# Performance work log

Hardware: AMD Instinct MI355X
Metric: run time of the kernel (lower is better)

The kernel has to match this reference:

```python
import jax, jax.numpy as jnp
import numpy as np
import math

B, T, C, H = 2, 2048, 1024, 16
HD = C // H  # head dim = 64

def setup_inputs() -> dict:
    key = jax.random.key(0)
    ks = jax.random.split(key, 12)
    s = 0.02
    return {
        "x": jax.random.normal(ks[0], (B, T, C), dtype=jnp.float32),
        "ln1_g": jnp.ones((C,), jnp.float32),
        "ln1_b": jnp.zeros((C,), jnp.float32),
        "W_attn": jax.random.normal(ks[1], (C, 3 * C), jnp.float32) * s,
        "b_attn": jnp.zeros((3 * C,), jnp.float32),
        "W_ap": jax.random.normal(ks[2], (C, C), jnp.float32) * s,
        "b_ap": jnp.zeros((C,), jnp.float32),
        "ln2_g": jnp.ones((C,), jnp.float32),
        "ln2_b": jnp.zeros((C,), jnp.float32),
        "W_fc": jax.random.normal(ks[3], (C, 4 * C), jnp.float32) * s,
        "b_fc": jnp.zeros((4 * C,), jnp.float32),
        "W_mp": jax.random.normal(ks[4], (4 * C, C), jnp.float32) * s,
        "b_mp": jnp.zeros((C,), jnp.float32),
    }

def layernorm(x, g, b, eps=1e-5):
    mu = jnp.mean(x, axis=-1, keepdims=True)
    var = jnp.mean(jnp.square(x - mu), axis=-1, keepdims=True)
    return (x - mu) * jax.lax.rsqrt(var + eps) * g + b

def gelu_tanh(x):
    # GELU(approximate='tanh')
    c = math.sqrt(2.0 / math.pi)
    return 0.5 * x * (1.0 + jnp.tanh(c * (x + 0.044715 * x * x * x)))

def attention(x, W_attn, b_attn, W_ap, b_ap):
    b, t, c = x.shape
    qkv = x @ W_attn + b_attn                      # [B,T,3C]
    q, k, v = jnp.split(qkv, 3, axis=-1)
    q = q.reshape(b, t, H, HD).transpose(0, 2, 1, 3)  # [B,H,T,hd]
    k = k.reshape(b, t, H, HD).transpose(0, 2, 1, 3)
    v = v.reshape(b, t, H, HD).transpose(0, 2, 1, 3)
    attn = jnp.einsum('bhqd,bhkd->bhqk', q, k) * (1.0 / math.sqrt(HD))
    mask = jnp.tril(jnp.ones((t, t), dtype=bool))
    attn = jnp.where(mask, attn, jnp.float32(-jnp.inf))
    attn = jax.nn.softmax(attn, axis=-1)
    y = jnp.einsum('bhqk,bhkd->bhqd', attn, v)
    y = y.transpose(0, 2, 1, 3).reshape(b, t, c)
    return y @ W_ap + b_ap

def reference(x, ln1_g, ln1_b, W_attn, b_attn, W_ap, b_ap,
              ln2_g, ln2_b, W_fc, b_fc, W_mp, b_mp):
    x = x + attention(layernorm(x, ln1_g, ln1_b), W_attn, b_attn, W_ap, b_ap)
    h = layernorm(x, ln2_g, ln2_b)
    h = gelu_tanh(h @ W_fc + b_fc) @ W_mp + b_mp
    return x + h
```

## Files before the change

### kernel.cpp

```cpp
#include <hip/hip_runtime.h>
#include <stdint.h>

#define TT_ 2048
#define CC_ 1024

typedef unsigned short u16;
typedef __bf16 bf16x8 __attribute__((ext_vector_type(8)));
typedef float f32x4 __attribute__((ext_vector_type(4)));
typedef unsigned short u16x8 __attribute__((ext_vector_type(8)));
typedef unsigned int u32x2 __attribute__((ext_vector_type(2)));

__device__ __forceinline__ u16 f2bf(float f) {
  unsigned u = __float_as_uint(f);
  u += 0x7fff + ((u >> 16) & 1);
  return (u16)(u >> 16);
}
__device__ __forceinline__ float bf2f(u16 v) {
  return __uint_as_float(((unsigned)v) << 16);
}

__device__ __forceinline__ float gelu_f(float t) {
  float u = 1.5957691216057308f * (t + 0.044715f * t * t * t);
  return t / (1.f + __expf(-u));
}

__device__ __forceinline__ void async_cp16(const u16* g, u16* l) {
  __builtin_amdgcn_global_load_lds(
      (const __attribute__((address_space(1))) void*)(uintptr_t)g,
      (__attribute__((address_space(3))) void*)(uint32_t)(uintptr_t)l,
      16, 0, 0);
}

__device__ __forceinline__ void blockbar() {
  asm volatile("" ::: "memory");
  __builtin_amdgcn_s_barrier();
  asm volatile("" ::: "memory");
}

__global__ __launch_bounds__(256) void kconv_t(const float* __restrict__ W,
                                               u16* __restrict__ WT, int K, int N) {
  __shared__ float t[32][33];
  int n0 = blockIdx.x * 32, k0 = blockIdx.y * 32;
  int tx = threadIdx.x & 31, ty = threadIdx.x >> 5;
#pragma unroll
  for (int r = 0; r < 4; ++r)
    t[ty + 8 * r][tx] = W[(size_t)(k0 + ty + 8 * r) * N + n0 + tx];
  __syncthreads();
#pragma unroll
  for (int r = 0; r < 4; ++r)
    WT[(size_t)(n0 + ty + 8 * r) * K + k0 + tx] = f2bf(t[tx][ty + 8 * r]);
}

__global__ __launch_bounds__(256) void kln(const float* __restrict__ x,
                                           const float* __restrict__ g,
                                           const float* __restrict__ b,
                                           u16* __restrict__ out) {
  int row = blockIdx.x, tid = threadIdx.x;
  const float4* xr = (const float4*)(x + (size_t)row * CC_);
  float4 v = xr[tid];
  float s = v.x + v.y + v.z + v.w;
  float s2 = v.x * v.x + v.y * v.y + v.z * v.z + v.w * v.w;
#pragma unroll
  for (int off = 32; off; off >>= 1) { s += __shfl_down(s, off); s2 += __shfl_down(s2, off); }
  __shared__ float rs[4], rq[4];
  int w = tid >> 6;
  if ((tid & 63) == 0) { rs[w] = s; rq[w] = s2; }
  __syncthreads();
  s = rs[0] + rs[1] + rs[2] + rs[3];
  s2 = rq[0] + rq[1] + rq[2] + rq[3];
  float mean = s * (1.f / CC_);
  float var = s2 * (1.f / CC_) - mean * mean;
  float rstd = rsqrtf(var + 1e-5f);
  float4 gv = ((const float4*)g)[tid];
  float4 bv = ((const float4*)b)[tid];
  u16* orow = out + (size_t)row * CC_ + tid * 4;
  orow[0] = f2bf((v.x - mean) * rstd * gv.x + bv.x);
  orow[1] = f2bf((v.y - mean) * rstd * gv.y + bv.y);
  orow[2] = f2bf((v.z - mean) * rstd * gv.z + bv.z);
  orow[3] = f2bf((v.w - mean) * rstd * gv.w + bv.w);
}

template <int EPI, int NSPLIT>
__global__ __launch_bounds__(256) void kgemm(const u16* __restrict__ A,
                                             const u16* __restrict__ BTm,
                                             const float* __restrict__ bias,
                                             const float* __restrict__ resid,
                                             void* __restrict__ out,
                                             float* __restrict__ part,
                                             int M, int N, int Ktot) {
  __shared__ __align__(16) u16 As[2][128 * 32];
  __shared__ __align__(16) u16 Bs[2][128 * 32];
  const int tid = threadIdx.x, lane = tid & 63, w = tid >> 6;
  const int llo = lane & 15, lhi = lane >> 4;
  const int row0 = blockIdx.y * 128, col0 = blockIdx.x * 128;
  const int wr = w >> 1, wc = w & 1;
  const int crow = lane >> 2;
  const int ck = (lane & 3) * 8;
  const int Kc = Ktot / NSPLIT;
  const int klo = (NSPLIT > 1) ? blockIdx.z * Kc : 0;

  f32x4 acc[4][4] = {};

  auto stage = [&](int bufi, int kof) {
#pragma unroll
    for (int c = w; c < 8; c += 4) {
      int r = c * 16 + crow;
      async_cp16(A + (size_t)(row0 + r) * Ktot + klo + kof + ck, &As[bufi][c * 512]);
      async_cp16(BTm + (size_t)(col0 + r) * Ktot + klo + kof + ck, &Bs[bufi][c * 512]);
    }
  };

  const int nt = Kc / 32;
  stage(0, 0);
  asm volatile("s_waitcnt vmcnt(0)" ::: "memory");
  blockbar();
  int cur = 0;

  for (int t = 0; t < nt; ++t) {
    if (t + 1 < nt) stage(cur ^ 1, (t + 1) * 32);
    bf16x8 af[4], bfr[4];
#pragma unroll
    for (int m = 0; m < 4; ++m)
      af[m] = *(const bf16x8*)&As[cur][(wr * 64 + m * 16 + llo) * 32 + lhi * 8];
#pragma unroll
    for (int n = 0; n < 4; ++n)
      bfr[n] = *(const bf16x8*)&Bs[cur][(wc * 64 + n * 16 + llo) * 32 + lhi * 8];
#pragma unroll
    for (int m = 0; m < 4; ++m)
#pragma unroll
      for (int n = 0; n < 4; ++n)
        acc[m][n] = __builtin_amdgcn_mfma_f32_16x16x32_bf16(af[m], bfr[n], acc[m][n], 0, 0, 0);
    if (t + 1 < nt) {
      asm volatile("s_waitcnt vmcnt(0)" ::: "memory");
      blockbar();
    }
    cur ^= 1;
  }

  const int c_row = row0 + wr * 64 + lhi * 4;
  const int c_col = col0 + wc * 64 + llo;
  const bool fin = (NSPLIT == 1) || (blockIdx.z == 0);
#pragma unroll
  for (int n = 0; n < 4; ++n) {
    int col = c_col + n * 16;
    float bb = bias[col];
#pragma unroll
    for (int m = 0; m < 4; ++m) {
      f32x4 a = acc[m][n];
#pragma unroll
      for (int i = 0; i < 4; ++i) {
        size_t idx = (size_t)(c_row + m * 16 + i) * N + col;
        if (!fin) {
          part[idx] = a[i];
        } else {
          float val = a[i] + bb;
          if constexpr (EPI == 1) {
            ((float*)out)[idx] = val + resid[idx];
          } else if constexpr (EPI == 2) {
            ((u16*)out)[idx] = f2bf(gelu_f(val));
          } else {
            ((u16*)out)[idx] = f2bf(val);
          }
        }
      }
    }
  }
}

template <int EPI, int NSPLIT>
__global__ __launch_bounds__(512, 2) void kgemm2(const u16* __restrict__ A,
                                                 const u16* __restrict__ BTm,
                                                 const float* __restrict__ bias,
                                                 const float* __restrict__ resid,
                                                 void* __restrict__ out,
                                                 u16* __restrict__ part,
                                                 int M, int N, int Ktot) {
  __shared__ __align__(16) u16 LB[4][2][8192];
  const int tid = threadIdx.x, lane = tid & 63, w = tid >> 6;
  const int llo = lane & 15, lhi = lane >> 4;
  const int wr = w >> 2, wc = w & 3;
  const int row0 = blockIdx.y * 256, col0 = blockIdx.x * 256;
  const int Kc = Ktot / NSPLIT;
  const int klo = (NSPLIT > 1) ? blockIdx.z * Kc : 0;
  const int nt = Kc / 32;

  const int wsA = w & 3;
  const int hbB = (wc >> 1);
  const int wsB = (w & 1) + ((w >> 2) << 1);

  const u16 *gA[2], *gB[2];
  int ldsA[2], ldsB[2];
#pragma unroll
  for (int l = 0; l < 2; ++l) {
    int c = l * 256 + wsA * 64 + lane;
    int rowl = c >> 2;
    int kc = ((c & 3) ^ ((c >> 3) & 3)) * 8;
    gA[l] = A + (size_t)(row0 + wr * 128 + rowl) * Ktot + klo + kc;
    ldsA[l] = wr * 4096 + (l * 256 + wsA * 64) * 8;
    int c2 = l * 256 + wsB * 64 + lane;
    int row2 = c2 >> 2;
    int kc2 = ((c2 & 3) ^ ((c2 >> 3) & 3)) * 8;
    gB[l] = BTm + (size_t)(col0 + hbB * 128 + row2) * Ktot + klo + kc2;
    ldsB[l] = hbB * 4096 + (l * 256 + wsB * 64) * 8;
  }

  auto stage = [&](int t) {
    int slot = t & 3;
#pragma unroll
    for (int l = 0; l < 2; ++l) {
      async_cp16(gA[l] + (size_t)t * 32, &LB[slot][0][ldsA[l]]);
      async_cp16(gB[l] + (size_t)t * 32, &LB[slot][1][ldsB[l]]);
    }
  };

  f32x4 acc[8][4] = {};
  for (int t = 0; t < 3 && t < nt; ++t) stage(t);
  const int swz = (llo >> 1) & 3;
  const int aoffb = wr * 4096 + llo * 32 + (lhi ^ swz) * 8;
  const int boffb = hbB * 4096 + ((wc & 1) * 64 + llo) * 32 + (lhi ^ swz) * 8;

  for (int t = 0; t < nt; ++t) {
    const int slot = t & 3;
    const int rem = nt - 1 - t;
    if (rem >= 2)      asm volatile("s_waitcnt vmcnt(8)" ::: "memory");
    else if (rem == 1) asm volatile("s_waitcnt vmcnt(4)" ::: "memory");
    else               asm volatile("s_waitcnt vmcnt(0)" ::: "memory");
    asm volatile("s_waitcnt lgkmcnt(0)" ::: "memory");
    blockbar();
    if (t + 3 < nt) stage(t + 3);

    bf16x8 af[8], bfv[4];
#pragma unroll
    for (int n = 0; n < 4; ++n)
      bfv[n] = *(const bf16x8*)&LB[slot][1][boffb + n * 512];
#pragma unroll
    for (int m = 0; m < 8; ++m)
      af[m] = *(const bf16x8*)&LB[slot][0][aoffb + m * 512];
    __builtin_amdgcn_s_setprio(1);
#pragma unroll
    for (int m = 0; m < 8; ++m)
#pragma unroll
      for (int n = 0; n < 4; ++n)
        acc[m][n] = __builtin_amdgcn_mfma_f32_16x16x32_bf16(af[m], bfv[n], acc[m][n], 0, 0, 0);
    __builtin_amdgcn_s_setprio(0);
  }

  const int c_row0 = row0 + wr * 128 + lhi * 4;
  const int c_col0 = col0 + wc * 64 + llo;
  const bool fin = (NSPLIT == 1) || (blockIdx.z == 0);
  u16* pb = part + (NSPLIT > 1 ? ((size_t)(blockIdx.z - 1)) * M * N : 0);
#pragma unroll
  for (int n = 0; n < 4; ++n) {
    int col = c_col0 + n * 16;
    float bb = bias[col];
#pragma unroll
    for (int m = 0; m < 8; ++m) {
      f32x4 a = acc[m][n];
#pragma unroll
      for (int i = 0; i < 4; ++i) {
        size_t idx = (size_t)(c_row0 + m * 16 + i) * N + col;
        if (!fin) {
          pb[idx] = f2bf(a[i]);
        } else {
          float val = a[i] + bb;
          if constexpr (EPI == 1) {
            ((float*)out)[idx] = val + resid[idx];
          } else if constexpr (EPI == 2) {
            ((u16*)out)[idx] = f2bf(gelu_f(val));
          } else {
            ((u16*)out)[idx] = f2bf(val);
          }
        }
      }
    }
  }
}

__global__ __launch_bounds__(256) void kadd3(float* __restrict__ out,
                                             const u16* __restrict__ p, size_t MN) {
  size_t i0 = ((size_t)blockIdx.x * 256 + threadIdx.x) * 8;
  float4 o0 = *(float4*)(out + i0);
  float4 o1 = *(float4*)(out + i0 + 4);
#pragma unroll
  for (int s = 0; s < 3; ++s) {
    u16x8 v = *(const u16x8*)(p + s * MN + i0);
    o0.x += bf2f(v[0]); o0.y += bf2f(v[1]); o0.z += bf2f(v[2]); o0.w += bf2f(v[3]);
    o1.x += bf2f(v[4]); o1.y += bf2f(v[5]); o1.z += bf2f(v[6]); o1.w += bf2f(v[7]);
  }
  *(float4*)(out + i0) = o0;
  *(float4*)(out + i0 + 4) = o1;
}

__global__ __launch_bounds__(256) void kvtrans(const u16* __restrict__ qkv,
                                               u16* __restrict__ VT) {
  int tt = blockIdx.x;
  int bh = blockIdx.y;
  int b = bh >> 4, h = bh & 15;
  __shared__ u16 t[64][72];
  int r = threadIdx.x >> 3, c0 = (threadIdx.x & 7) * 8;
  const u16* src = qkv + (size_t)(b * TT_ + tt * 64) * 3072 + 2048 + h * 64;
#pragma unroll
  for (int it = 0; it < 2; ++it) {
    int rr = r + it * 32;
    *(u16x8*)&t[rr][c0] = *(const u16x8*)(src + (size_t)rr * 3072 + c0);
  }
  __syncthreads();
  u16* dst = VT + ((size_t)bh * 64) * TT_ + tt * 64;
#pragma unroll
  for (int it = 0; it < 2; ++it) {
    int d = r + it * 32;
    u16x8 v;
#pragma unroll
    for (int e = 0; e < 8; ++e) v[e] = t[c0 + e][d];
    *(u16x8*)(dst + (size_t)d * TT_ + c0) = v;
  }
}

__global__ __launch_bounds__(512, 4) void kattn(const u16* __restrict__ qkv,
                                                const u16* __restrict__ VT,
                                                u16* __restrict__ y) {
  const int h = blockIdx.x, b = blockIdx.y;
  const int z = blockIdx.z;
  const int qt = (z < 8) ? (15 - z) : (z - 8);
  const int tid = threadIdx.x, lane = tid & 63, w = tid >> 6;
  const int llo = lane & 15, lhi = lane >> 4;

  __shared__ __align__(16) u16 Qs[128 * 64];
  __shared__ __align__(16) u16 Ks[2][64 * 64];
  __shared__ __align__(16) u16 Vs[2][64 * 64];
  __shared__ __align__(16) u16 Ps[128 * 72];

  const size_t tok0 = (size_t)b * TT_;
  const int q0 = qt * 128;
  const u16* qb = qkv + tok0 * 3072 + h * 64;
  const u16* kb = qb + 1024;

  {
    const float alpha = 0.18033688011112042f;
    int r8 = tid >> 3, ce = (tid & 7) * 8;
#pragma unroll
    for (int it = 0; it < 2; ++it) {
      int tk = it * 64 + r8;
      u16x8 v = *(const u16x8*)(qb + (size_t)(q0 + tk) * 3072 + ce);
#pragma unroll
      for (int e = 0; e < 8; ++e) v[e] = f2bf(bf2f(v[e]) * alpha);
      *(u16x8*)&Qs[tk * 64 + (ce ^ ((tk & 7) << 3))] = v;
    }
  }
  asm volatile("s_waitcnt lgkmcnt(0)" ::: "memory");

  const int p_ = w * 8 + (lane >> 3);
  const int krow = ((p_ & 15) << 2) | (p_ >> 4);
  const int scol = ((lane & 7) * 8) ^ ((p_ & 7) << 3);
  const u16* kg = kb + (size_t)krow * 3072 + scol;
  const u16* vg = VT + ((size_t)(b * 16 + h) * 64 + p_) * TT_ + scol;

  const int ntiles = 2 * qt + 2;
  async_cp16(kg, &Ks[0][w * 512]);
  async_cp16(vg, &Vs[0][w * 512]);

  blockbar();

  bf16x8 aq[2];
#pragma unroll
  for (int kk = 0; kk < 2; ++kk)
    aq[kk] = *(const bf16x8*)&Qs[(w * 16 + llo) * 64 + ((kk * 32 + lhi * 8) ^ ((llo & 7) << 3))];

  float m_i[4], l_i[4];
  f32x4 o[4] = {};
#pragma unroll
  for (int i = 0; i < 4; ++i) { m_i[i] = -1e30f; l_i[i] = 0.f; }

  const int row_min = q0 + w * 16, row_max = row_min + 15;
  int buf = 0;

  for (int j = 0; j < ntiles; ++j) {
    if (j + 1 < ntiles) {
      async_cp16(kg + (size_t)(j + 1) * (64 * 3072), &Ks[buf ^ 1][w * 512]);
      async_cp16(vg + (size_t)(j + 1) * 64, &Vs[buf ^ 1][w * 512]);
      asm volatile("s_waitcnt vmcnt(2)" ::: "memory");
    } else {
      asm volatile("s_waitcnt vmcnt(0)" ::: "memory");
    }
    blockbar();

    const int kmin = j * 64;
    if (kmin <= row_max) {
      f32x4 s[4] = {};
      __builtin_amdgcn_s_setprio(1);
#pragma unroll
      for (int nb = 0; nb < 4; ++nb)
#pragma unroll
        for (int kk = 0; kk < 2; ++kk) {
          bf16x8 bk = *(const bf16x8*)&Ks[buf][(nb * 16 + llo) * 64 +
                                              ((kk * 32 + lhi * 8) ^ ((llo & 7) << 3))];
          s[nb] = __builtin_amdgcn_mfma_f32_16x16x32_bf16(aq[kk], bk, s[nb], 0, 0, 0);
        }
      __builtin_amdgcn_s_setprio(0);

      const bool part = (kmin + 63 > row_min);
      float sc[4][4];
#pragma unroll
      for (int nb = 0; nb < 4; ++nb)
#pragma unroll
        for (int i = 0; i < 4; ++i) {
          float v = s[nb][i];
          if (part && (kmin + llo * 4 + nb > row_min + lhi * 4 + i)) v = -1e30f;
          sc[nb][i] = v;
        }

      float rm[4];
#pragma unroll
      for (int i = 0; i < 4; ++i) {
        float r = fmaxf(fmaxf(sc[0][i], sc[1][i]), fmaxf(sc[2][i], sc[3][i]));
#pragma unroll
        for (int off = 1; off < 16; off <<= 1) r = fmaxf(r, __shfl_xor(r, off));
        rm[i] = r;
      }

      bool need = (rm[0] > m_i[0] + 8.f) | (rm[1] > m_i[1] + 8.f) |
                  (rm[2] > m_i[2] + 8.f) | (rm[3] > m_i[3] + 8.f);
      if (__any(need)) {
#pragma unroll
        for (int i = 0; i < 4; ++i) {
          float mn = fmaxf(m_i[i], rm[i]);
          float corr = exp2f(m_i[i] - mn);
          l_i[i] *= corr;
#pragma unroll
          for (int db = 0; db < 4; ++db) o[db][i] *= corr;
          m_i[i] = mn;
        }
      }

#pragma unroll
      for (int i = 0; i < 4; ++i) {
        float p0 = exp2f(sc[0][i] - m_i[i]);
        float p1 = exp2f(sc[1][i] - m_i[i]);
        float p2 = exp2f(sc[2][i] - m_i[i]);
        float p3 = exp2f(sc[3][i] - m_i[i]);
        float rsum = (p0 + p1) + (p2 + p3);
#pragma unroll
        for (int off = 1; off < 16; off <<= 1) rsum += __shfl_xor(rsum, off);
        l_i[i] += rsum;
        u32x2 pk;
        pk[0] = (unsigned)f2bf(p0) | ((unsigned)f2bf(p1) << 16);
        pk[1] = (unsigned)f2bf(p2) | ((unsigned)f2bf(p3) << 16);
        *(u32x2*)&Ps[(w * 16 + lhi * 4 + i) * 72 + llo * 4] = pk;
      }

      bf16x8 pa[2];
#pragma unroll
      for (int kk = 0; kk < 2; ++kk)
        pa[kk] = *(const bf16x8*)&Ps[(w * 16 + llo) * 72 + kk * 32 + lhi * 8];
      __builtin_amdgcn_s_setprio(1);
#pragma unroll
      for (int db = 0; db < 4; ++db)
#pragma unroll
        for (int kk = 0; kk < 2; ++kk) {
          bf16x8 bv = *(const bf16x8*)&Vs[buf][(db * 16 + llo) * 64 +
                                              ((kk * 32 + lhi * 8) ^ ((llo & 7) << 3))];
          o[db] = __builtin_amdgcn_mfma_f32_16x16x32_bf16(pa[kk], bv, o[db], 0, 0, 0);
        }
      __builtin_amdgcn_s_setprio(0);
    }
    blockbar();
    buf ^= 1;
  }

#pragma unroll
  for (int i = 0; i < 4; ++i) {
    float inv = 1.f / l_i[i];
    size_t row = tok0 + q0 + w * 16 + lhi * 4 + i;
#pragma unroll
    for (int db = 0; db < 4; ++db)
      y[row * CC_ + h * 64 + db * 16 + llo] = f2bf(o[db][i] * inv);
  }
}

extern "C" void kernel_launch(void* const* d_in, const int* in_sizes, int n_in,
                              void* d_out, int out_size, void* d_ws, size_t ws_size,
                              hipStream_t stream) {
  (void)in_sizes; (void)n_in; (void)out_size; (void)ws_size;
  const float* x      = (const float*)d_in[0];
  const float* ln1g   = (const float*)d_in[1];
  const float* ln1b   = (const float*)d_in[2];
  const float* W_attn = (const float*)d_in[3];
  const float* b_attn = (const float*)d_in[4];
  const float* W_ap   = (const float*)d_in[5];
  const float* b_ap   = (const float*)d_in[6];
  const float* ln2g   = (const float*)d_in[7];
  const float* ln2b   = (const float*)d_in[8];
  const float* W_fc   = (const float*)d_in[9];
  const float* b_fc   = (const float*)d_in[10];
  const float* W_mp   = (const float*)d_in[11];
  const float* b_mp   = (const float*)d_in[12];

  char* p = (char*)d_ws;
  u16* WTmp   = (u16*)p; p += (size_t)4096 * 1024 * 2;
  u16* WTattn = (u16*)p; p += (size_t)3072 * 1024 * 2;
  u16* WTap   = (u16*)p; p += (size_t)1024 * 1024 * 2;
  u16* WTfc   = (u16*)p; p += (size_t)4096 * 1024 * 2;
  u16* xn     = (u16*)p; p += (size_t)4096 * 1024 * 2;
  u16* qkvb   = (u16*)p; p += (size_t)4096 * 3072 * 2;
  u16* yb     = (u16*)p; p += (size_t)4096 * 1024 * 2;
  float* x1   = (float*)p; p += (size_t)4096 * 1024 * 4;
  u16* h2     = (u16*)p; p += (size_t)4096 * 1024 * 2;
  u16* fcb    = qkvb;
  u16* VT     = (u16*)x1;
  u16* mpp    = WTattn;

  kconv_t<<<dim3(96, 32), 256, 0, stream>>>(W_attn, WTattn, 1024, 3072);
  kconv_t<<<dim3(32, 32), 256, 0, stream>>>(W_ap, WTap, 1024, 1024);
  kconv_t<<<dim3(128, 32), 256, 0, stream>>>(W_fc, WTfc, 1024, 4096);
  kconv_t<<<dim3(32, 128), 256, 0, stream>>>(W_mp, WTmp, 4096, 1024);

  kln<<<4096, 256, 0, stream>>>(x, ln1g, ln1b, xn);
  kgemm2<0, 1><<<dim3(12, 16), 512, 0, stream>>>(xn, WTattn, b_attn, nullptr, qkvb, nullptr, 4096, 3072, 1024);
  kvtrans<<<dim3(32, 32), 256, 0, stream>>>(qkvb, VT);
  kattn<<<dim3(16, 2, 16), 512, 0, stream>>>(qkvb, VT, yb);
  kgemm<1, 1><<<dim3(8, 32), 256, 0, stream>>>(yb, WTap, b_ap, x, x1, nullptr, 4096, 1024, 1024);
  kln<<<4096, 256, 0, stream>>>(x1, ln2g, ln2b, h2);
  kgemm2<2, 1><<<dim3(16, 16), 512, 0, stream>>>(h2, WTfc, b_fc, nullptr, fcb, nullptr, 4096, 4096, 1024);
  kgemm2<1, 4><<<dim3(4, 16, 4), 512, 0, stream>>>(fcb, WTmp, b_mp, x1, (float*)d_out, mpp, 4096, 1024, 4096);
  kadd3<<<2048, 256, 0, stream>>>((float*)d_out, mpp, (size_t)4096 * 1024);
}
```

Before: 283.0 us.

## Restructure causal attention into paired 64-row q-tiles per block and swap QKV GEMM

The attention kernel now uses 256-thread blocks that each process two 64-row query tiles (z and 31-z), so every block does the same amount of causal work. Masking is applied only on the diagonal tile, which drops the per-tile partial-mask checks and the skipped-tile branch. Row-sum shuffles move out of the inner loop and run once at the end, and P is packed to bf16 with a native vector conversion. The QKV projection switches from kgemm2 to the smaller-tile kgemm with a larger grid. Risks include less K/V reuse per block and a different GEMM efficiency profile.

```diff
diff --git a/kernel.cpp b/kernel.cpp
--- a/kernel.cpp
+++ b/kernel.cpp
@@ -6,9 +6,9 @@
 
 typedef unsigned short u16;
 typedef __bf16 bf16x8 __attribute__((ext_vector_type(8)));
+typedef __bf16 bf16x4 __attribute__((ext_vector_type(4)));
 typedef float f32x4 __attribute__((ext_vector_type(4)));
 typedef unsigned short u16x8 __attribute__((ext_vector_type(8)));
-typedef unsigned int u32x2 __attribute__((ext_vector_type(2)));
 
 __device__ __forceinline__ u16 f2bf(float f) {
   unsigned u = __float_as_uint(f);
@@ -316,76 +316,80 @@
   }
 }
 
-__global__ __launch_bounds__(512, 4) void kattn(const u16* __restrict__ qkv,
+__global__ __launch_bounds__(256, 4) void kattn(const u16* __restrict__ qkv,
                                                 const u16* __restrict__ VT,
                                                 u16* __restrict__ y) {
-  const int h = blockIdx.x, b = blockIdx.y;
-  const int z = blockIdx.z;
-  const int qt = (z < 8) ? (15 - z) : (z - 8);
+  const int h = blockIdx.x, b = blockIdx.y, z = blockIdx.z;
   const int tid = threadIdx.x, lane = tid & 63, w = tid >> 6;
   const int llo = lane & 15, lhi = lane >> 4;
 
-  __shared__ __align__(16) u16 Qs[128 * 64];
+  __shared__ __align__(16) u16 Qs[64 * 64];
   __shared__ __align__(16) u16 Ks[2][64 * 64];
   __shared__ __align__(16) u16 Vs[2][64 * 64];
-  __shared__ __align__(16) u16 Ps[128 * 72];
+  __shared__ __align__(16) u16 Ps[64 * 72];
 
   const size_t tok0 = (size_t)b * TT_;
-  const int q0 = qt * 128;
   const u16* qb = qkv + tok0 * 3072 + h * 64;
   const u16* kb = qb + 1024;
 
-  {
-    const float alpha = 0.18033688011112042f;
-    int r8 = tid >> 3, ce = (tid & 7) * 8;
+  const u16 *kg[2], *vg[2];
+#pragma unroll
+  for (int it = 0; it < 2; ++it) {
+    int p_ = w * 16 + it * 8 + (lane >> 3);
+    int krow = ((p_ & 15) << 2) | (p_ >> 4);
+    int scol = ((lane & 7) * 8) ^ ((p_ & 7) << 3);
+    kg[it] = kb + (size_t)krow * 3072 + scol;
+    vg[it] = VT + ((size_t)(b * 16 + h) * 64 + p_) * TT_ + scol;
+  }
+
+  auto stageKV = [&](int bufi, int j) {
+    async_cp16(kg[0] + (size_t)j * (64 * 3072), &Ks[bufi][(w * 16 + 0) * 64]);
+    async_cp16(kg[1] + (size_t)j * (64 * 3072), &Ks[bufi][(w * 16 + 8) * 64]);
+    async_cp16(vg[0] + (size_t)j * 64, &Vs[bufi][(w * 16 + 0) * 64]);
+    async_cp16(vg[1] + (size_t)j * 64, &Vs[bufi][(w * 16 + 8) * 64]);
+  };
+
+  const float alpha = 0.18033688011112042f;
+  const int r8 = tid >> 3, ce = (tid & 7) * 8;
+
+#pragma unroll 1
+  for (int ph = 0; ph < 2; ++ph) {
+    const int qt = ph ? (31 - z) : z;
+    const int q0 = qt * 64;
+
 #pragma unroll
     for (int it = 0; it < 2; ++it) {
-      int tk = it * 64 + r8;
+      int tk = it * 32 + r8;
       u16x8 v = *(const u16x8*)(qb + (size_t)(q0 + tk) * 3072 + ce);
 #pragma unroll
       for (int e = 0; e < 8; ++e) v[e] = f2bf(bf2f(v[e]) * alpha);
       *(u16x8*)&Qs[tk * 64 + (ce ^ ((tk & 7) << 3))] = v;
     }
-  }
-  asm volatile("s_waitcnt lgkmcnt(0)" ::: "memory");
-
-  const int p_ = w * 8 + (lane >> 3);
-  const int krow = ((p_ & 15) << 2) | (p_ >> 4);
-  const int scol = ((lane & 7) * 8) ^ ((p_ & 7) << 3);
-  const u16* kg = kb + (size_t)krow * 3072 + scol;
-  const u16* vg = VT + ((size_t)(b * 16 + h) * 64 + p_) * TT_ + scol;
-
-  const int ntiles = 2 * qt + 2;
-  async_cp16(kg, &Ks[0][w * 512]);
-  async_cp16(vg, &Vs[0][w * 512]);
-
-  blockbar();
-
-  bf16x8 aq[2];
-#pragma unroll
-  for (int kk = 0; kk < 2; ++kk)
-    aq[kk] = *(const bf16x8*)&Qs[(w * 16 + llo) * 64 + ((kk * 32 + lhi * 8) ^ ((llo & 7) << 3))];
-
-  float m_i[4], l_i[4];
-  f32x4 o[4] = {};
-#pragma unroll
-  for (int i = 0; i < 4; ++i) { m_i[i] = -1e30f; l_i[i] = 0.f; }
-
-  const int row_min = q0 + w * 16, row_max = row_min + 15;
-  int buf = 0;
-
-  for (int j = 0; j < ntiles; ++j) {
-    if (j + 1 < ntiles) {
-      async_cp16(kg + (size_t)(j + 1) * (64 * 3072), &Ks[buf ^ 1][w * 512]);
-      async_cp16(vg + (size_t)(j + 1) * 64, &Vs[buf ^ 1][w * 512]);
-      asm volatile("s_waitcnt vmcnt(2)" ::: "memory");
-    } else {
-      asm volatile("s_waitcnt vmcnt(0)" ::: "memory");
-    }
+    asm volatile("s_waitcnt lgkmcnt(0)" ::: "memory");
+    stageKV(0, 0);
     blockbar();
 
-    const int kmin = j * 64;
-    if (kmin <= row_max) {
+    bf16x8 aq[2];
+#pragma unroll
+    for (int kk = 0; kk < 2; ++kk)
+      aq[kk] = *(const bf16x8*)&Qs[(w * 16 + llo) * 64 +
+                                   ((kk * 32 + lhi * 8) ^ ((llo & 7) << 3))];
+
+    float m_i[4], l_i[4];
+    f32x4 o[4] = {};
+#pragma unroll
+    for (int i = 0; i < 4; ++i) { m_i[i] = -1e30f; l_i[i] = 0.f; }
+
+    int buf = 0;
+    for (int j = 0; j <= qt; ++j) {
+      if (j < qt) {
+        stageKV(buf ^ 1, j + 1);
+        asm volatile("s_waitcnt vmcnt(4)" ::: "memory");
+      } else {
+        asm volatile("s_waitcnt vmcnt(0)" ::: "memory");
+      }
+      blockbar();
+
       f32x4 s[4] = {};
       __builtin_amdgcn_s_setprio(1);
 #pragma unroll
@@ -398,16 +402,22 @@
         }
       __builtin_amdgcn_s_setprio(0);
 
-      const bool part = (kmin + 63 > row_min);
       float sc[4][4];
-#pragma unroll
-      for (int nb = 0; nb < 4; ++nb)
-#pragma unroll
-        for (int i = 0; i < 4; ++i) {
-          float v = s[nb][i];
-          if (part && (kmin + llo * 4 + nb > row_min + lhi * 4 + i)) v = -1e30f;
-          sc[nb][i] = v;
-        }
+      if (j == qt) {
+#pragma unroll
+        for (int nb = 0; nb < 4; ++nb)
+#pragma unroll
+          for (int i = 0; i < 4; ++i) {
+            float v = s[nb][i];
+            if (llo * 4 + nb > w * 16 + lhi * 4 + i) v = -1e30f;
+            sc[nb][i] = v;
+          }
+      } else {
+#pragma unroll
+        for (int nb = 0; nb < 4; ++nb)
+#pragma unroll
+          for (int i = 0; i < 4; ++i) sc[nb][i] = s[nb][i];
+      }
 
       float rm[4];
 #pragma unroll
@@ -438,14 +448,9 @@
         float p1 = exp2f(sc[1][i] - m_i[i]);
         float p2 = exp2f(sc[2][i] - m_i[i]);
         float p3 = exp2f(sc[3][i] - m_i[i]);
-        float rsum = (p0 + p1) + (p2 + p3);
-#pragma unroll
-        for (int off = 1; off < 16; off <<= 1) rsum += __shfl_xor(rsum, off);
-        l_i[i] += rsum;
-        u32x2 pk;
-        pk[0] = (unsigned)f2bf(p0) | ((unsigned)f2bf(p1) << 16);
-        pk[1] = (unsigned)f2bf(p2) | ((unsigned)f2bf(p3) << 16);
-        *(u32x2*)&Ps[(w * 16 + lhi * 4 + i) * 72 + llo * 4] = pk;
+        l_i[i] += (p0 + p1) + (p2 + p3);
+        bf16x4 pk = {(__bf16)p0, (__bf16)p1, (__bf16)p2, (__bf16)p3};
+        *(bf16x4*)&Ps[(w * 16 + lhi * 4 + i) * 72 + llo * 4] = pk;
       }
 
       bf16x8 pa[2];
@@ -462,18 +467,21 @@
           o[db] = __builtin_amdgcn_mfma_f32_16x16x32_bf16(pa[kk], bv, o[db], 0, 0, 0);
         }
       __builtin_amdgcn_s_setprio(0);
-    }
-    blockbar();
-    buf ^= 1;
-  }
-
-#pragma unroll
-  for (int i = 0; i < 4; ++i) {
-    float inv = 1.f / l_i[i];
-    size_t row = tok0 + q0 + w * 16 + lhi * 4 + i;
-#pragma unroll
-    for (int db = 0; db < 4; ++db)
-      y[row * CC_ + h * 64 + db * 16 + llo] = f2bf(o[db][i] * inv);
+      blockbar();
+      buf ^= 1;
+    }
+
+#pragma unroll
+    for (int i = 0; i < 4; ++i) {
+      float t = l_i[i];
+#pragma unroll
+      for (int off = 1; off < 16; off <<= 1) t += __shfl_xor(t, off);
+      float inv = 1.f / t;
+      size_t row = tok0 + q0 + w * 16 + lhi * 4 + i;
+#pragma unroll
+      for (int db = 0; db < 4; ++db)
+        y[row * CC_ + h * 64 + db * 16 + llo] = f2bf(o[db][i] * inv);
+    }
   }
 }
 
@@ -515,9 +523,9 @@
   kconv_t<<<dim3(32, 128), 256, 0, stream>>>(W_mp, WTmp, 4096, 1024);
 
   kln<<<4096, 256, 0, stream>>>(x, ln1g, ln1b, xn);
-  kgemm2<0, 1><<<dim3(12, 16), 512, 0, stream>>>(xn, WTattn, b_attn, nullptr, qkvb, nullptr, 4096, 3072, 1024);
+  kgemm<0, 1><<<dim3(24, 32), 256, 0, stream>>>(xn, WTattn, b_attn, nullptr, qkvb, nullptr, 4096, 3072, 1024);
   kvtrans<<<dim3(32, 32), 256, 0, stream>>>(qkvb, VT);
-  kattn<<<dim3(16, 2, 16), 512, 0, stream>>>(qkvb, VT, yb);
+  kattn<<<dim3(16, 2, 16), 256, 0, stream>>>(qkvb, VT, yb);
   kgemm<1, 1><<<dim3(8, 32), 256, 0, stream>>>(yb, WTap, b_ap, x, x1, nullptr, 4096, 1024, 1024);
   kln<<<4096, 256, 0, stream>>>(x1, ln2g, ln2b, h2);
   kgemm2<2, 1><<<dim3(16, 16), 512, 0, stream>>>(h2, WTfc, b_fc, nullptr, fcb, nullptr, 4096, 4096, 1024);
```

After: 273.8 us. 3.3% less time.
